# Optimization experiments

Measured on AMD Instinct MI355X. Metric: run time of the kernel, lower is better.

Reference implementation:

```python
import jax, jax.numpy as jnp
import numpy as np

# Architecture search space (matches init_kwargs)
IN_DIMS = (512, 768, 1024)
OUT_MULTS = (2, 3, 4)
MAX_IN = max(IN_DIMS)                       # 1024
MAX_OUT = max(IN_DIMS) * max(OUT_MULTS)     # 4096


def _masks():
    # k iterates (i over IN_DIMS, j over OUT_MULTS) in row-major order, matching
    # the original double loop. Slicing weight[:out_dim, :in_dim] then zero-padding
    # to [MAX_OUT, MAX_IN] is equivalent to multiplying by rank-1 mask
    # row_mask[k] (x) col_mask[k].
    out_dims = np.array([m * i for i in IN_DIMS for m in OUT_MULTS])  # [K=9]
    in_dims = np.array([i for i in IN_DIMS for _ in OUT_MULTS])       # [K=9]
    row_mask = (np.arange(MAX_OUT)[None, :] < out_dims[:, None]).astype(np.float32)  # [K, MAX_OUT]
    col_mask = (np.arange(MAX_IN)[None, :] < in_dims[:, None]).astype(np.float32)    # [K, MAX_IN]
    return jnp.asarray(row_mask), jnp.asarray(col_mask)


def setup_inputs() -> dict:
    key = jax.random.key(0)
    k1, k2, k3, k4 = jax.random.split(key, 4)
    x = jax.random.normal(k1, (8, 4096, MAX_IN), dtype=jnp.float32)
    weights = jax.random.uniform(k2, (9,), dtype=jnp.float32)  # mixing coefficients
    W = jax.random.normal(k3, (MAX_OUT, MAX_IN), dtype=jnp.float32) * 0.02  # linear_layer.weight
    b = jax.random.normal(k4, (MAX_OUT,), dtype=jnp.float32) * 0.02         # linear_layer.bias
    return {"x": x, "weights": weights, "W": W, "b": b}


def reference(x, weights, W, b):
    # weights_mix = sum_k weights[k] * pad(W[:o_k, :i_k]) = W * coeff, where
    # coeff[o, i] = sum_k weights[k] * row_mask[k, o] * col_mask[k, i].
    row_mask, col_mask = _masks()
    coeff = jnp.einsum('k,ko,ki->oi', weights, row_mask, col_mask)  # [MAX_OUT, MAX_IN]
    W_mix = W * coeff
    b_mix = b * (weights @ row_mask)                                # [MAX_OUT]
    # F.linear: y = x @ W_mix.T + b_mix
    return jnp.einsum('bsi,oi->bso', x, W_mix) + b_mix
```

## Files before the change

kernel.cpp:

```cpp
#include <hip/hip_runtime.h>

#define KDIM 1024
#define NDIM 4096

typedef __attribute__((ext_vector_type(4))) float f32x4;
typedef __attribute__((ext_vector_type(8))) short s16x8;
typedef __attribute__((ext_vector_type(8))) unsigned short u16x8;

__device__ __forceinline__ unsigned short f2bf(float f) {
    union { float f; unsigned u; } v; v.f = f;
    unsigned r = v.u + 0x7FFFu + ((v.u >> 16) & 1u);
    return (unsigned short)(r >> 16);
}

#define GLDS(gsrc, ldst)                                                        \
    __builtin_amdgcn_global_load_lds(                                           \
        (const __attribute__((address_space(1))) unsigned int*)(gsrc),          \
        (__attribute__((address_space(3))) unsigned int*)(ldst), 16, 0, 0)

#define SBAR() __builtin_amdgcn_s_barrier()
#define VMW(n) asm volatile("s_waitcnt vmcnt(" #n ")" ::: "memory")
#define LGKM0() asm volatile("s_waitcnt lgkmcnt(0)" ::: "memory")

__device__ __forceinline__ void row_coeffs(int o, const float* w,
                                           float& rp0, float& rp1, float& rp2) {
    rp2 = (o < 2048 ? w[6] : 0.f) + (o < 3072 ? w[7] : 0.f) + w[8];
    rp1 = rp2 + (o < 1536 ? w[3] : 0.f) + (o < 2304 ? w[4] : 0.f) + (o < 3072 ? w[5] : 0.f);
    rp0 = rp1 + (o < 1024 ? w[0] : 0.f) + (o < 1536 ? w[1] : 0.f) + (o < 2048 ? w[2] : 0.f);
}

__device__ __forceinline__ float row_bias_coef(int n, const float* w) {
    return (n < 1024 ? w[0] : 0.f) + (n < 1536 ? w[1] : 0.f)
         + (n < 2048 ? w[2] : 0.f) + (n < 1536 ? w[3] : 0.f)
         + (n < 2304 ? w[4] : 0.f) + (n < 3072 ? w[5] : 0.f)
         + (n < 2048 ? w[6] : 0.f) + (n < 3072 ? w[7] : 0.f) + w[8];
}

__global__ __launch_bounds__(256) void prep_x(const float* __restrict__ X,
                                              unsigned short* __restrict__ XB, int n8) {
    int i = blockIdx.x * blockDim.x + threadIdx.x;
    const int stride = gridDim.x * blockDim.x;
    for (; i < n8; i += stride) {
        const f32x4* p = (const f32x4*)(X + (size_t)i * 8);
        f32x4 a = p[0], b = p[1];
        u16x8 o;
        o[0] = f2bf(a[0]); o[1] = f2bf(a[1]); o[2] = f2bf(a[2]); o[3] = f2bf(a[3]);
        o[4] = f2bf(b[0]); o[5] = f2bf(b[1]); o[6] = f2bf(b[2]); o[7] = f2bf(b[3]);
        *(u16x8*)(XB + (size_t)i * 8) = o;
    }
}

__global__ __launch_bounds__(256) void prep_w(const float* __restrict__ W,
                                              const float* __restrict__ wts,
                                              unsigned short* __restrict__ WB) {
    const int g = blockIdx.x * blockDim.x + threadIdx.x;
    if (g >= NDIM * (KDIM / 8)) return;
    const int o = g >> 7, ig = g & 127;
    float w[9];
#pragma unroll
    for (int k = 0; k < 9; ++k) w[k] = wts[k];
    float rp0, rp1, rp2;
    row_coeffs(o, w, rp0, rp1, rp2);
    const float cf = ig < 64 ? rp0 : (ig < 96 ? rp1 : rp2);
    const f32x4* p = (const f32x4*)(W + (size_t)g * 8);
    f32x4 a = p[0], b = p[1];
    u16x8 ov;
    ov[0] = f2bf(a[0] * cf); ov[1] = f2bf(a[1] * cf); ov[2] = f2bf(a[2] * cf); ov[3] = f2bf(a[3] * cf);
    ov[4] = f2bf(b[0] * cf); ov[5] = f2bf(b[1] * cf); ov[6] = f2bf(b[2] * cf); ov[7] = f2bf(b[3] * cf);
    *(u16x8*)(WB + (size_t)g * 8) = ov;
}

__global__ __launch_bounds__(512, 2) void mlv2_gemm_v7(
    const unsigned short* __restrict__ XB,
    const unsigned short* __restrict__ WB,
    const float* __restrict__ wts,
    const float* __restrict__ bias,
    float* __restrict__ Y)
{
    __shared__ unsigned short LDS[4 * 16384];

    const int tid = (int)threadIdx.x;
    const int l   = tid & 63;
    const int w   = tid >> 6;
    const int wm  = w >> 2;
    const int wn  = w & 3;

    const int bid = (int)blockIdx.x;
    const int xcd = bid & 7;
    const int i   = bid >> 3;
    const int n_tile = xcd * 2 + (i & 1);
    const int m_tile = i >> 1;
    const int m0 = m_tile * 256;
    const int n0 = n_tile * 256;

    const int rl = l & 15;
    const unsigned cw = (unsigned)((((l >> 4) ^ ((l >> 1) & 3)) * 8));
    unsigned offA[8], offB[4];
#pragma unroll
    for (int m = 0; m < 8; ++m)
        offA[m] = (unsigned)((wm * 128 + m * 16 + rl) * 32) + cw;
#pragma unroll
    for (int n = 0; n < 4; ++n)
        offB[n] = 8192u + (unsigned)((wn * 64 + n * 16 + rl) * 32) + cw;

    const int cg = (((l & 3) ^ ((l >> 3) & 3)) * 8);
    const int r0 = w * 32 + (l >> 2);
    const unsigned short* sA0 = XB + (size_t)(m0 + r0) * KDIM + cg;
    const unsigned short* sA1 = XB + (size_t)(m0 + r0 + 16) * KDIM + cg;
    const unsigned short* sB0 = WB + (size_t)(n0 + r0) * KDIM + cg;
    const unsigned short* sB1 = WB + (size_t)(n0 + r0 + 16) * KDIM + cg;
    const unsigned dA0 = (unsigned)(w * 1024);
    const unsigned dA1 = dA0 + 512;
    const unsigned dB0 = 8192u + dA0;
    const unsigned dB1 = 8192u + dA1;

    auto stage = [&](int buf, int kt) {
        const int ko = kt * 32;
        const unsigned ob = (unsigned)buf * 16384u;
        GLDS(sA0 + ko, &LDS[ob + dA0]);
        GLDS(sA1 + ko, &LDS[ob + dA1]);
        GLDS(sB0 + ko, &LDS[ob + dB0]);
        GLDS(sB1 + ko, &LDS[ob + dB1]);
    };

    f32x4 acc[8][4];
#pragma unroll
    for (int m = 0; m < 8; ++m)
#pragma unroll
        for (int n = 0; n < 4; ++n) acc[m][n] = (f32x4){0.f, 0.f, 0.f, 0.f};

    auto compute = [&](int buf) {
        const unsigned short* base = &LDS[(unsigned)buf * 16384u];
        s16x8 af[8], bfr[4];
#pragma unroll
        for (int n = 0; n < 4; ++n) bfr[n] = *(const s16x8*)(base + offB[n]);
#pragma unroll
        for (int m = 0; m < 8; ++m) af[m] = *(const s16x8*)(base + offA[m]);
        __builtin_amdgcn_s_setprio(1);
#pragma unroll
        for (int m = 0; m < 8; ++m)
#pragma unroll
            for (int n = 0; n < 4; ++n)
                acc[m][n] = __builtin_amdgcn_mfma_f32_16x16x32_bf16(
                    af[m], bfr[n], acc[m][n], 0, 0, 0);
        __builtin_amdgcn_s_setprio(0);
    };

    stage(0, 0); stage(1, 1); stage(2, 2);
    VMW(8);
    SBAR();

    for (int kt = 0; kt < 29; ++kt) {
        stage((kt + 3) & 3, kt + 3);
        compute(kt & 3);
        VMW(8); LGKM0(); SBAR();
    }
    compute(29 & 3);
    VMW(4); LGKM0(); SBAR();
    compute(30 & 3);
    VMW(0); LGKM0(); SBAR();
    compute(31 & 3);

    float w9[9];
#pragma unroll
    for (int k = 0; k < 9; ++k) w9[k] = wts[k];
    const int gmb = m0 + wm * 128 + (l >> 4) * 4;
    const int gnb = n0 + wn * 64 + rl;
#pragma unroll
    for (int n = 0; n < 4; ++n) {
        const int gn = gnb + n * 16;
        const float bc = bias[gn] * row_bias_coef(gn, w9);
#pragma unroll
        for (int m = 0; m < 8; ++m) {
            float* yp = Y + (size_t)(gmb + m * 16) * NDIM + gn;
            yp[0 * NDIM] = acc[m][n][0] + bc;
            yp[1 * NDIM] = acc[m][n][1] + bc;
            yp[2 * NDIM] = acc[m][n][2] + bc;
            yp[3 * NDIM] = acc[m][n][3] + bc;
        }
    }
}

__global__ __launch_bounds__(256, 2) void mlv2_gemm_v1(
    const float* __restrict__ X, const float* __restrict__ wts,
    const float* __restrict__ W, const float* __restrict__ bias,
    float* __restrict__ Y)
{
    __shared__ unsigned short Alds[2][4][128][8];
    __shared__ unsigned short Blds[2][4][128][8];
    const int tid = (int)threadIdx.x;
    const int bid = (int)blockIdx.x;
    const int wg  = (bid & 7) * 1024 + (bid >> 3);
    const int n_tile = wg & 31;
    const int m_tile = wg >> 5;
    float w[9];
#pragma unroll
    for (int k = 0; k < 9; ++k) w[k] = wts[k];
    const int srow = tid >> 1;
    const int scol = (tid & 1) << 4;
    const int kc0  = (tid & 1) << 1;
    const float* xp = X + (size_t)(m_tile * 128 + srow) * KDIM + scol;
    const float* wp = W + (size_t)(n_tile * 128 + srow) * KDIM + scol;
    const int orow = n_tile * 128 + srow;
    float rp0, rp1, rp2;
    row_coeffs(orow, w, rp0, rp1, rp2);
    const int lane = tid & 63, wv = tid >> 6;
    const int frow = lane & 15, kcl = lane >> 4;
    const int arow0 = (wv >> 1) * 64 + frow;
    const int brow0 = (wv & 1) * 64 + frow;
    auto coef = [&](int t) -> float { return t < 16 ? rp0 : (t < 24 ? rp1 : rp2); };
    auto stage_load = [&](int t, f32x4 a[4], f32x4 b[4]) {
        const f32x4* xq = (const f32x4*)(xp + t * 32);
        const f32x4* wq = (const f32x4*)(wp + t * 32);
#pragma unroll
        for (int j = 0; j < 4; ++j) { a[j] = xq[j]; b[j] = wq[j]; }
    };
    auto stage_write = [&](int buf, const f32x4 a[4], const f32x4 b[4], float cf) {
        u16x8 va[2], vb[2];
#pragma unroll
        for (int j = 0; j < 4; ++j)
#pragma unroll
            for (int e = 0; e < 4; ++e) {
                const int idx = j * 4 + e;
                va[idx >> 3][idx & 7] = f2bf(a[j][e]);
                vb[idx >> 3][idx & 7] = f2bf(b[j][e] * cf);
            }
        *(u16x8*)&Alds[buf][kc0    ][srow][0] = va[0];
        *(u16x8*)&Alds[buf][kc0 + 1][srow][0] = va[1];
        *(u16x8*)&Blds[buf][kc0    ][srow][0] = vb[0];
        *(u16x8*)&Blds[buf][kc0 + 1][srow][0] = vb[1];
    };
    f32x4 acc[4][4];
#pragma unroll
    for (int i = 0; i < 4; ++i)
#pragma unroll
        for (int j = 0; j < 4; ++j) acc[i][j] = (f32x4){0.f, 0.f, 0.f, 0.f};
    {
        f32x4 a[4], b[4];
        stage_load(0, a, b);
        stage_write(0, a, b, coef(0));
    }
    __syncthreads();
    const int NT = KDIM / 32;
    int cur = 0;
    for (int t = 0; t < NT; ++t) {
        f32x4 a[4], b[4];
        if (t + 1 < NT) stage_load(t + 1, a, b);
        s16x8 af[4], bf_[4];
#pragma unroll
        for (int i = 0; i < 4; ++i) {
            af[i]  = *(const s16x8*)&Alds[cur][kcl][arow0 + i * 16][0];
            bf_[i] = *(const s16x8*)&Blds[cur][kcl][brow0 + i * 16][0];
        }
#pragma unroll
        for (int i = 0; i < 4; ++i)
#pragma unroll
            for (int j = 0; j < 4; ++j)
                acc[i][j] = __builtin_amdgcn_mfma_f32_16x16x32_bf16(
                    af[i], bf_[j], acc[i][j], 0, 0, 0);
        if (t + 1 < NT) stage_write(cur ^ 1, a, b, coef(t + 1));
        __syncthreads();
        cur ^= 1;
    }
    const int gm0 = m_tile * 128 + (wv >> 1) * 64 + kcl * 4;
    const int gn0 = n_tile * 128 + (wv & 1) * 64 + frow;
#pragma unroll
    for (int j = 0; j < 4; ++j) {
        const int n = gn0 + j * 16;
        const float bc = bias[n] * row_bias_coef(n, w);
#pragma unroll
        for (int i = 0; i < 4; ++i) {
            float* yp = Y + (size_t)(gm0 + i * 16) * NDIM + n;
            yp[0 * NDIM] = acc[i][j][0] + bc;
            yp[1 * NDIM] = acc[i][j][1] + bc;
            yp[2 * NDIM] = acc[i][j][2] + bc;
            yp[3 * NDIM] = acc[i][j][3] + bc;
        }
    }
}

extern "C" void kernel_launch(void* const* d_in, const int* in_sizes, int n_in,
                              void* d_out, int out_size, void* d_ws, size_t ws_size,
                              hipStream_t stream) {
    const float* X    = (const float*)d_in[0];
    const float* wts  = (const float*)d_in[1];
    const float* W    = (const float*)d_in[2];
    const float* bias = (const float*)d_in[3];
    float* Y = (float*)d_out;

    const int M = in_sizes[0] / KDIM;

    const size_t xb_elems = (size_t)M * KDIM;
    const size_t wb_elems = (size_t)NDIM * KDIM;
    const size_t ws_needed = (xb_elems + wb_elems) * sizeof(unsigned short);

    if (ws_size >= ws_needed && (M % 256) == 0) {
        unsigned short* XB = (unsigned short*)d_ws;
        unsigned short* WB = XB + xb_elems;
        prep_x<<<4096, 256, 0, stream>>>(X, XB, (int)(xb_elems / 8));
        prep_w<<<(NDIM * (KDIM / 8)) / 256, 256, 0, stream>>>(W, wts, WB);
        const int grid = (M / 256) * (NDIM / 256);
        mlv2_gemm_v7<<<grid, 512, 0, stream>>>(XB, WB, wts, bias, Y);
    } else {
        const int grid = (M / 128) * (NDIM / 128);
        mlv2_gemm_v1<<<grid, 256, 0, stream>>>(X, wts, W, bias, Y);
    }
}
```

Before: 396.0 us.

## Switch GEMM to 4-wave 32x32x16 MFMA with register double-buffered LDS reads

```diff
diff --git a/kernel.cpp b/kernel.cpp
--- a/kernel.cpp
+++ b/kernel.cpp
@@ -4,6 +4,7 @@
 #define NDIM 4096
 
 typedef __attribute__((ext_vector_type(4))) float f32x4;
+typedef __attribute__((ext_vector_type(16))) float f32x16;
 typedef __attribute__((ext_vector_type(8))) short s16x8;
 typedef __attribute__((ext_vector_type(8))) unsigned short u16x8;
 
@@ -20,7 +21,6 @@
 
 #define SBAR() __builtin_amdgcn_s_barrier()
 #define VMW(n) asm volatile("s_waitcnt vmcnt(" #n ")" ::: "memory")
-#define LGKM0() asm volatile("s_waitcnt lgkmcnt(0)" ::: "memory")
 
 __device__ __forceinline__ void row_coeffs(int o, const float* w,
                                            float& rp0, float& rp1, float& rp2) {
@@ -70,7 +70,7 @@
     *(u16x8*)(WB + (size_t)g * 8) = ov;
 }
 
-__global__ __launch_bounds__(512, 2) void mlv2_gemm_v7(
+__global__ __launch_bounds__(256, 1) void mlv2_gemm_v8(
     const unsigned short* __restrict__ XB,
     const unsigned short* __restrict__ WB,
     const float* __restrict__ wts,
@@ -82,8 +82,8 @@
     const int tid = (int)threadIdx.x;
     const int l   = tid & 63;
     const int w   = tid >> 6;
-    const int wm  = w >> 2;
-    const int wn  = w & 3;
+    const int wm  = w >> 1;
+    const int wn  = w & 1;
 
     const int bid = (int)blockIdx.x;
     const int xcd = bid & 7;
@@ -93,90 +93,114 @@
     const int m0 = m_tile * 256;
     const int n0 = n_tile * 256;
 
-    const int rl = l & 15;
-    const unsigned cw = (unsigned)((((l >> 4) ^ ((l >> 1) & 3)) * 8));
-    unsigned offA[8], offB[4];
-#pragma unroll
-    for (int m = 0; m < 8; ++m)
-        offA[m] = (unsigned)((wm * 128 + m * 16 + rl) * 32) + cw;
-#pragma unroll
-    for (int n = 0; n < 4; ++n)
-        offB[n] = 8192u + (unsigned)((wn * 64 + n * 16 + rl) * 32) + cw;
-
-    const int cg = (((l & 3) ^ ((l >> 3) & 3)) * 8);
-    const int r0 = w * 32 + (l >> 2);
-    const unsigned short* sA0 = XB + (size_t)(m0 + r0) * KDIM + cg;
-    const unsigned short* sA1 = XB + (size_t)(m0 + r0 + 16) * KDIM + cg;
-    const unsigned short* sB0 = WB + (size_t)(n0 + r0) * KDIM + cg;
-    const unsigned short* sB1 = WB + (size_t)(n0 + r0 + 16) * KDIM + cg;
-    const unsigned dA0 = (unsigned)(w * 1024);
-    const unsigned dA1 = dA0 + 512;
-    const unsigned dB0 = 8192u + dA0;
-    const unsigned dB1 = 8192u + dA1;
-
-    auto stage = [&](int buf, int kt) {
+    unsigned offA[4][2], offB[4][2];
+#pragma unroll
+    for (int mt = 0; mt < 4; ++mt)
+#pragma unroll
+        for (int ks = 0; ks < 2; ++ks) {
+            const unsigned kg = (unsigned)(ks * 2 + (l >> 5));
+            offA[mt][ks] = (kg * 256 + (unsigned)(wm * 128 + mt * 32 + (l & 31))) * 8u;
+            offB[mt][ks] = 8192u + (kg * 256 + (unsigned)(wn * 128 + mt * 32 + (l & 31))) * 8u;
+        }
+
+    const unsigned short* sA[4];
+    const unsigned short* sB[4];
+    unsigned dstA[4], dstB[4];
+#pragma unroll
+    for (int q = 0; q < 4; ++q) {
+        sA[q] = XB + (size_t)(m0 + w * 64 + l) * KDIM + q * 8;
+        sB[q] = WB + (size_t)(n0 + w * 64 + l) * KDIM + q * 8;
+        dstA[q] = (unsigned)((q * 256 + w * 64) * 8);
+        dstB[q] = 8192u + dstA[q];
+    }
+
+    auto stage = [&](int kt) {
+        const unsigned bb = (unsigned)(kt & 3) * 16384u;
         const int ko = kt * 32;
-        const unsigned ob = (unsigned)buf * 16384u;
-        GLDS(sA0 + ko, &LDS[ob + dA0]);
-        GLDS(sA1 + ko, &LDS[ob + dA1]);
-        GLDS(sB0 + ko, &LDS[ob + dB0]);
-        GLDS(sB1 + ko, &LDS[ob + dB1]);
-    };
-
-    f32x4 acc[8][4];
-#pragma unroll
-    for (int m = 0; m < 8; ++m)
-#pragma unroll
-        for (int n = 0; n < 4; ++n) acc[m][n] = (f32x4){0.f, 0.f, 0.f, 0.f};
-
-    auto compute = [&](int buf) {
-        const unsigned short* base = &LDS[(unsigned)buf * 16384u];
-        s16x8 af[8], bfr[4];
-#pragma unroll
-        for (int n = 0; n < 4; ++n) bfr[n] = *(const s16x8*)(base + offB[n]);
-#pragma unroll
-        for (int m = 0; m < 8; ++m) af[m] = *(const s16x8*)(base + offA[m]);
+#pragma unroll
+        for (int q = 0; q < 4; ++q) {
+            GLDS(sA[q] + ko, &LDS[bb + dstA[q]]);
+            GLDS(sB[q] + ko, &LDS[bb + dstB[q]]);
+        }
+    };
+
+    f32x16 acc[4][4];
+#pragma unroll
+    for (int mt = 0; mt < 4; ++mt)
+#pragma unroll
+        for (int nt = 0; nt < 4; ++nt)
+#pragma unroll
+            for (int r = 0; r < 16; ++r) acc[mt][nt][r] = 0.f;
+
+    s16x8 aX[4][2], bX[4][2], aY[4][2], bY[4][2];
+
+    auto rd = [&](s16x8 (&a)[4][2], s16x8 (&b)[4][2], int kt) {
+        const unsigned bb = (unsigned)(kt & 3) * 16384u;
+#pragma unroll
+        for (int mt = 0; mt < 4; ++mt)
+#pragma unroll
+            for (int ks = 0; ks < 2; ++ks) {
+                a[mt][ks] = *(const s16x8*)&LDS[bb + offA[mt][ks]];
+                b[mt][ks] = *(const s16x8*)&LDS[bb + offB[mt][ks]];
+            }
+    };
+    auto mm = [&](const s16x8 (&a)[4][2], const s16x8 (&b)[4][2]) {
         __builtin_amdgcn_s_setprio(1);
 #pragma unroll
-        for (int m = 0; m < 8; ++m)
-#pragma unroll
-            for (int n = 0; n < 4; ++n)
-                acc[m][n] = __builtin_amdgcn_mfma_f32_16x16x32_bf16(
-                    af[m], bfr[n], acc[m][n], 0, 0, 0);
+        for (int ks = 0; ks < 2; ++ks)
+#pragma unroll
+            for (int mt = 0; mt < 4; ++mt)
+#pragma unroll
+                for (int nt = 0; nt < 4; ++nt)
+                    acc[mt][nt] = __builtin_amdgcn_mfma_f32_32x32x16_bf16(
+                        a[mt][ks], b[nt][ks], acc[mt][nt], 0, 0, 0);
         __builtin_amdgcn_s_setprio(0);
     };
 
-    stage(0, 0); stage(1, 1); stage(2, 2);
+    stage(0); stage(1); stage(2);
     VMW(8);
     SBAR();
-
-    for (int kt = 0; kt < 29; ++kt) {
-        stage((kt + 3) & 3, kt + 3);
-        compute(kt & 3);
-        VMW(8); LGKM0(); SBAR();
-    }
-    compute(29 & 3);
-    VMW(4); LGKM0(); SBAR();
-    compute(30 & 3);
-    VMW(0); LGKM0(); SBAR();
-    compute(31 & 3);
+    rd(aX, bX, 0);
+
+    for (int kt = 0; kt < 28; kt += 2) {
+        rd(aY, bY, kt + 1);
+        stage(kt + 3);
+        mm(aX, bX);
+        VMW(8); SBAR();
+
+        rd(aX, bX, kt + 2);
+        stage(kt + 4);
+        mm(aY, bY);
+        VMW(8); SBAR();
+    }
+    rd(aY, bY, 29);
+    stage(31);
+    mm(aX, bX);
+    VMW(8); SBAR();
+    rd(aX, bX, 30);
+    mm(aY, bY);
+    VMW(0); SBAR();
+    rd(aY, bY, 31);
+    mm(aX, bX);
+    mm(aY, bY);
 
     float w9[9];
 #pragma unroll
     for (int k = 0; k < 9; ++k) w9[k] = wts[k];
-    const int gmb = m0 + wm * 128 + (l >> 4) * 4;
-    const int gnb = n0 + wn * 64 + rl;
-#pragma unroll
-    for (int n = 0; n < 4; ++n) {
-        const int gn = gnb + n * 16;
+    const int colb = l & 31;
+    const int rhi  = (l >> 5) * 4;
+#pragma unroll
+    for (int nt = 0; nt < 4; ++nt) {
+        const int gn = n0 + wn * 128 + nt * 32 + colb;
         const float bc = bias[gn] * row_bias_coef(gn, w9);
 #pragma unroll
-        for (int m = 0; m < 8; ++m) {
-            float* yp = Y + (size_t)(gmb + m * 16) * NDIM + gn;
-            yp[0 * NDIM] = acc[m][n][0] + bc;
-            yp[1 * NDIM] = acc[m][n][1] + bc;
-            yp[2 * NDIM] = acc[m][n][2] + bc;
-            yp[3 * NDIM] = acc[m][n][3] + bc;
+        for (int mt = 0; mt < 4; ++mt) {
+            const int rb = m0 + wm * 128 + mt * 32 + rhi;
+#pragma unroll
+            for (int r = 0; r < 16; ++r) {
+                const int row = rb + (r & 3) + 8 * (r >> 2);
+                Y[(size_t)row * NDIM + gn] = acc[mt][nt][r] + bc;
+            }
         }
     }
 }
@@ -300,7 +324,7 @@
         prep_x<<<4096, 256, 0, stream>>>(X, XB, (int)(xb_elems / 8));
         prep_w<<<(NDIM * (KDIM / 8)) / 256, 256, 0, stream>>>(W, wts, WB);
         const int grid = (M / 256) * (NDIM / 256);
-        mlv2_gemm_v7<<<grid, 512, 0, stream>>>(XB, WB, wts, bias, Y);
+        mlv2_gemm_v8<<<grid, 256, 0, stream>>>(XB, WB, wts, bias, Y);
     } else {
         const int grid = (M / 128) * (NDIM / 128);
         mlv2_gemm_v1<<<grid, 256, 0, stream>>>(X, wts, W, bias, Y);
```

Result: slower. 637.6 us (+61.0%).

## Pre-pack X and W into tile-contiguous swizzled bf16 panels for GEMM

Applied to the files above, without the earlier changes.

```diff
diff --git a/kernel.cpp b/kernel.cpp
--- a/kernel.cpp
+++ b/kernel.cpp
@@ -36,41 +36,53 @@
          + (n < 2048 ? w[6] : 0.f) + (n < 3072 ? w[7] : 0.f) + w[8];
 }
 
-__global__ __launch_bounds__(256) void prep_x(const float* __restrict__ X,
-                                              unsigned short* __restrict__ XB, int n8) {
-    int i = blockIdx.x * blockDim.x + threadIdx.x;
-    const int stride = gridDim.x * blockDim.x;
-    for (; i < n8; i += stride) {
-        const f32x4* p = (const f32x4*)(X + (size_t)i * 8);
-        f32x4 a = p[0], b = p[1];
-        u16x8 o;
-        o[0] = f2bf(a[0]); o[1] = f2bf(a[1]); o[2] = f2bf(a[2]); o[3] = f2bf(a[3]);
-        o[4] = f2bf(b[0]); o[5] = f2bf(b[1]); o[6] = f2bf(b[2]); o[7] = f2bf(b[3]);
-        *(u16x8*)(XB + (size_t)i * 8) = o;
-    }
-}
-
-__global__ __launch_bounds__(256) void prep_w(const float* __restrict__ W,
-                                              const float* __restrict__ wts,
-                                              unsigned short* __restrict__ WB) {
-    const int g = blockIdx.x * blockDim.x + threadIdx.x;
-    if (g >= NDIM * (KDIM / 8)) return;
-    const int o = g >> 7, ig = g & 127;
+__global__ __launch_bounds__(256) void prep_x_p(const float* __restrict__ X,
+                                                unsigned short* __restrict__ XB,
+                                                int nchunks) {
+    const int g = blockIdx.x * 256 + threadIdx.x;
+    if (g >= nchunks) return;
+    const int c   = g & 1023;
+    const int p   = g >> 10;
+    const int kt  = p & 31;
+    const int mt  = p >> 5;
+    const int row = c >> 2;
+    const int kcl = (c & 3) ^ ((row >> 1) & 3);
+    const float* src = X + ((size_t)(mt * 256 + row) * KDIM + kt * 32 + kcl * 8);
+    f32x4 a = *(const f32x4*)src, b = *(const f32x4*)(src + 4);
+    u16x8 o;
+    o[0] = f2bf(a[0]); o[1] = f2bf(a[1]); o[2] = f2bf(a[2]); o[3] = f2bf(a[3]);
+    o[4] = f2bf(b[0]); o[5] = f2bf(b[1]); o[6] = f2bf(b[2]); o[7] = f2bf(b[3]);
+    *(u16x8*)(XB + (size_t)g * 8) = o;
+}
+
+__global__ __launch_bounds__(256) void prep_w_p(const float* __restrict__ W,
+                                                const float* __restrict__ wts,
+                                                unsigned short* __restrict__ WB,
+                                                int nchunks) {
+    const int g = blockIdx.x * 256 + threadIdx.x;
+    if (g >= nchunks) return;
+    const int c   = g & 1023;
+    const int p   = g >> 10;
+    const int kt  = p & 31;
+    const int nt  = p >> 5;
+    const int row = c >> 2;
+    const int kcl = (c & 3) ^ ((row >> 1) & 3);
     float w[9];
 #pragma unroll
     for (int k = 0; k < 9; ++k) w[k] = wts[k];
     float rp0, rp1, rp2;
-    row_coeffs(o, w, rp0, rp1, rp2);
-    const float cf = ig < 64 ? rp0 : (ig < 96 ? rp1 : rp2);
-    const f32x4* p = (const f32x4*)(W + (size_t)g * 8);
-    f32x4 a = p[0], b = p[1];
-    u16x8 ov;
-    ov[0] = f2bf(a[0] * cf); ov[1] = f2bf(a[1] * cf); ov[2] = f2bf(a[2] * cf); ov[3] = f2bf(a[3] * cf);
-    ov[4] = f2bf(b[0] * cf); ov[5] = f2bf(b[1] * cf); ov[6] = f2bf(b[2] * cf); ov[7] = f2bf(b[3] * cf);
-    *(u16x8*)(WB + (size_t)g * 8) = ov;
-}
-
-__global__ __launch_bounds__(512, 2) void mlv2_gemm_v7(
+    row_coeffs(nt * 256 + row, w, rp0, rp1, rp2);
+    const int i0 = kt * 32 + kcl * 8;
+    const float cf = i0 < 512 ? rp0 : (i0 < 768 ? rp1 : rp2);
+    const float* src = W + ((size_t)(nt * 256 + row) * KDIM + i0);
+    f32x4 a = *(const f32x4*)src, b = *(const f32x4*)(src + 4);
+    u16x8 o;
+    o[0] = f2bf(a[0] * cf); o[1] = f2bf(a[1] * cf); o[2] = f2bf(a[2] * cf); o[3] = f2bf(a[3] * cf);
+    o[4] = f2bf(b[0] * cf); o[5] = f2bf(b[1] * cf); o[6] = f2bf(b[2] * cf); o[7] = f2bf(b[3] * cf);
+    *(u16x8*)(WB + (size_t)g * 8) = o;
+}
+
+__global__ __launch_bounds__(512, 2) void mlv2_gemm_v9(
     const unsigned short* __restrict__ XB,
     const unsigned short* __restrict__ WB,
     const float* __restrict__ wts,
@@ -94,33 +106,30 @@
     const int n0 = n_tile * 256;
 
     const int rl = l & 15;
-    const unsigned cw = (unsigned)((((l >> 4) ^ ((l >> 1) & 3)) * 8));
+    const unsigned swz = (unsigned)((l >> 4) ^ ((rl >> 1) & 3));
     unsigned offA[8], offB[4];
 #pragma unroll
     for (int m = 0; m < 8; ++m)
-        offA[m] = (unsigned)((wm * 128 + m * 16 + rl) * 32) + cw;
+        offA[m] = ((unsigned)(wm * 128 + m * 16 + rl) * 4u + swz) * 8u;
 #pragma unroll
     for (int n = 0; n < 4; ++n)
-        offB[n] = 8192u + (unsigned)((wn * 64 + n * 16 + rl) * 32) + cw;
-
-    const int cg = (((l & 3) ^ ((l >> 3) & 3)) * 8);
-    const int r0 = w * 32 + (l >> 2);
-    const unsigned short* sA0 = XB + (size_t)(m0 + r0) * KDIM + cg;
-    const unsigned short* sA1 = XB + (size_t)(m0 + r0 + 16) * KDIM + cg;
-    const unsigned short* sB0 = WB + (size_t)(n0 + r0) * KDIM + cg;
-    const unsigned short* sB1 = WB + (size_t)(n0 + r0 + 16) * KDIM + cg;
+        offB[n] = 8192u + ((unsigned)(wn * 64 + n * 16 + rl) * 4u + swz) * 8u;
+
+    const unsigned cA0 = (unsigned)(w * 128 + l) * 8u;
+    const unsigned cA1 = cA0 + 512u;
     const unsigned dA0 = (unsigned)(w * 1024);
-    const unsigned dA1 = dA0 + 512;
+    const unsigned dA1 = dA0 + 512u;
     const unsigned dB0 = 8192u + dA0;
     const unsigned dB1 = 8192u + dA1;
 
     auto stage = [&](int buf, int kt) {
-        const int ko = kt * 32;
+        const unsigned short* pa = XB + ((size_t)(m_tile * 32 + kt) << 13);
+        const unsigned short* pb = WB + ((size_t)(n_tile * 32 + kt) << 13);
         const unsigned ob = (unsigned)buf * 16384u;
-        GLDS(sA0 + ko, &LDS[ob + dA0]);
-        GLDS(sA1 + ko, &LDS[ob + dA1]);
-        GLDS(sB0 + ko, &LDS[ob + dB0]);
-        GLDS(sB1 + ko, &LDS[ob + dB1]);
+        GLDS(pa + cA0, &LDS[ob + dA0]);
+        GLDS(pa + cA1, &LDS[ob + dA1]);
+        GLDS(pb + cA0, &LDS[ob + dB0]);
+        GLDS(pb + cA1, &LDS[ob + dB1]);
     };
 
     f32x4 acc[8][4];
@@ -297,10 +306,12 @@
     if (ws_size >= ws_needed && (M % 256) == 0) {
         unsigned short* XB = (unsigned short*)d_ws;
         unsigned short* WB = XB + xb_elems;
-        prep_x<<<4096, 256, 0, stream>>>(X, XB, (int)(xb_elems / 8));
-        prep_w<<<(NDIM * (KDIM / 8)) / 256, 256, 0, stream>>>(W, wts, WB);
+        const int xchunks = (int)(xb_elems / 8);
+        const int wchunks = (int)(wb_elems / 8);
+        prep_x_p<<<(xchunks + 255) / 256, 256, 0, stream>>>(X, XB, xchunks);
+        prep_w_p<<<(wchunks + 255) / 256, 256, 0, stream>>>(W, wts, WB, wchunks);
         const int grid = (M / 256) * (NDIM / 256);
-        mlv2_gemm_v7<<<grid, 512, 0, stream>>>(XB, WB, wts, bias, Y);
+        mlv2_gemm_v9<<<grid, 512, 0, stream>>>(XB, WB, wts, bias, Y);
     } else {
         const int grid = (M / 128) * (NDIM / 128);
         mlv2_gemm_v1<<<grid, 256, 0, stream>>>(X, wts, W, bias, Y);
```

After: 377.6 us. 1.05x faster.
